# Optimization experiments

Measured on AMD Instinct MI355X. Metric: run time of the kernel, lower is better.

## Reference

```python
import jax, jax.numpy as jnp
import numpy as np

B, Cin, Cout, H, W = 8, 64, 128, 128, 128
K, S, P = 3, 1, 1
KK = K * K
EPS = 1e-5


def _conv2d(x, w, b=None):
    out = jax.lax.conv_general_dilated(
        x, w, window_strides=(S, S), padding=[(P, P), (P, P)],
        dimension_numbers=('NCHW', 'OIHW', 'NCHW'))
    if b is not None:
        out = out + b[None, :, None, None]
    return out


def setup_inputs() -> dict:
    key = jax.random.key(0)
    k = jax.random.split(key, 5)
    sc = 1.0 / np.sqrt(Cin * KK)
    return {
        'x': jax.random.normal(k[0], (B, Cin, H, W), jnp.float32),
        'offset_w': jax.random.normal(k[1], (2 * KK, Cin, K, K), jnp.float32) * sc,
        'offset_b': jnp.zeros((2 * KK,), jnp.float32),
        'mask_w': jax.random.normal(k[2], (KK, Cin, K, K), jnp.float32) * sc,
        'mask_b': jnp.zeros((KK,), jnp.float32),
        'conv_w': jax.random.normal(k[3], (Cout, Cin, K, K), jnp.float32) * sc,
    }


def _deform_conv2d(x, offset, mask, w):
    """Modulated deformable conv (torchvision deform_conv2d semantics)."""
    Bn, C, Hh, Ww = x.shape
    Ho, Wo = offset.shape[2], offset.shape[3]
    off = offset.reshape(Bn, KK, 2, Ho, Wo)  # (y, x) pairs per kernel tap
    ky, kx = jnp.meshgrid(jnp.arange(K), jnp.arange(K), indexing='ij')
    ky = ky.reshape(KK).astype(x.dtype)
    kx = kx.reshape(KK).astype(x.dtype)
    hy = (jnp.arange(Ho) * S - P).astype(x.dtype)
    wx = (jnp.arange(Wo) * S - P).astype(x.dtype)
    # sampling positions [B, KK, Ho, Wo]
    py = off[:, :, 0] + ky[None, :, None, None] + hy[None, None, :, None]
    px = off[:, :, 1] + kx[None, :, None, None] + wx[None, None, None, :]

    y0 = jnp.floor(py)
    x0 = jnp.floor(px)
    wy1 = py - y0; wx1 = px - x0
    wy0 = 1.0 - wy1; wx0 = 1.0 - wx1

    xf = x.reshape(Bn, C, Hh * Ww)

    def gather(yi, xi):
        valid = ((yi >= 0) & (yi < Hh) & (xi >= 0) & (xi < Ww)).astype(x.dtype)
        yc = jnp.clip(yi, 0, Hh - 1).astype(jnp.int32)
        xc = jnp.clip(xi, 0, Ww - 1).astype(jnp.int32)
        idx = (yc * Ww + xc).reshape(Bn, -1)  # [B, KK*Ho*Wo]
        vals = jnp.take_along_axis(xf, idx[:, None, :], axis=2)  # [B, C, KK*Ho*Wo]
        return vals.reshape(Bn, C, KK, Ho, Wo) * valid.reshape(Bn, 1, KK, Ho, Wo)

    v = (gather(y0, x0) * (wy0 * wx0)[:, None]
         + gather(y0, x0 + 1) * (wy0 * wx1)[:, None]
         + gather(y0 + 1, x0) * (wy1 * wx0)[:, None]
         + gather(y0 + 1, x0 + 1) * (wy1 * wx1)[:, None])  # [B, C, KK, Ho, Wo]
    v = v * mask[:, None]  # modulation
    return jnp.einsum('bckhw,ock->bohw', v, w.reshape(w.shape[0], C, KK))


def reference(x, offset_w, offset_b, mask_w, mask_b, conv_w):
    offset = _conv2d(x, offset_w, offset_b)
    mask = jax.nn.sigmoid(_conv2d(x, mask_w, mask_b))
    out = _deform_conv2d(x, offset, mask, conv_w)
    # BatchNorm2d(affine=False), training-mode normalization over (N, H, W)
    mean = out.mean(axis=(0, 2, 3), keepdims=True)
    var = out.var(axis=(0, 2, 3), keepdims=True)
    return jax.nn.relu((out - mean) * jax.lax.rsqrt(var + EPS))
```

## Files before the change

kernel.cpp:

```cpp
#include <hip/hip_runtime.h>
#include <hip/hip_bf16.h>

#define H_ 128
#define W_ 128
#define HW 16384
#define CIN 64
#define COUT 128
#define KK9 9
#define BATCH 8
#define NPIX (BATCH * HW)
#define KDIM 576

typedef short bf16x8 __attribute__((ext_vector_type(8)));
typedef float f32x4  __attribute__((ext_vector_type(4)));
typedef unsigned short ushort_t;

union U4B { uint4 u; bf16x8 v; };

__device__ __forceinline__ float us2f(unsigned short u) {
    unsigned int v = ((unsigned int)u) << 16;
    float f;
    __builtin_memcpy(&f, &v, 4);
    return f;
}
__device__ __forceinline__ float lo_f(unsigned int w) {
    unsigned int v = w << 16;
    float f;
    __builtin_memcpy(&f, &v, 4);
    return f;
}
__device__ __forceinline__ float hi_f(unsigned int w) {
    unsigned int v = w & 0xffff0000u;
    float f;
    __builtin_memcpy(&f, &v, 4);
    return f;
}
__device__ __forceinline__ unsigned short f2us_bf(float f) {
    __hip_bfloat16 h = __float2bfloat16(f);
    unsigned short u;
    __builtin_memcpy(&u, &h, 2);
    return u;
}
__device__ __forceinline__ unsigned int pack2(float a, float b) {
    return (unsigned int)f2us_bf(a) | ((unsigned int)f2us_bf(b) << 16);
}

template <bool F32>
__device__ __forceinline__ float ld_in(const void* p, long i) {
    if (F32) return ((const float*)p)[i];
    return us2f(((const unsigned short*)p)[i]);
}

__global__ void detect_zero(const uint4* __restrict__ xr4,
                            float* __restrict__ flag,
                            float* __restrict__ gstat) {
    int t = threadIdx.x;
#pragma unroll
    for (int i = 0; i < 16; ++i) gstat[i * 256 + t] = 0.0f;
    if (t < 64) {
        uint4 v = xr4[t];
        unsigned int w[4] = {v.x, v.y, v.z, v.w};
        int big = 0;
#pragma unroll
        for (int q = 0; q < 4; ++q) {
            big += (((w[q] >> 7)  & 0xFF) >= 0xC0);
            big += (((w[q] >> 23) & 0xFF) >= 0xC0);
        }
        unsigned long long m = __ballot(big > 0);
        if (t == 0) flag[0] = m ? 1.0f : 0.0f;
    }
}

template <bool F32>
__device__ __forceinline__ void prep_body(const void* offw, const void* offb,
                                          const void* maskw, const void* maskb,
                                          const void* convw,
                                          ushort_t* wTs, ushort_t* wcats,
                                          float* bias, int i) {
    if (i < 73728) {
        int j = i & 7, lane = (i >> 3) & 63, n = (i >> 9) & 7, ks = i >> 12;
        int co = n * 16 + (lane & 15);
        int k  = ks * 32 + ((lane >> 4) << 3) + j;
        int kk = k >> 6, ci = k & 63;
        wTs[i] = f2us_bf(ld_in<F32>(convw, (long)co * KDIM + ci * 9 + kk));
    } else if (i < 73728 + 18432) {
        int i2 = i - 73728;
        int j = i2 & 7, lane = (i2 >> 3) & 63, n = (i2 >> 9) & 1, ks = i2 >> 10;
        int co2 = n * 16 + (lane & 15);
        int k   = ks * 32 + ((lane >> 4) << 3) + j;
        int kk = k >> 6, ci = k & 63;
        float v = 0.0f;
        if (co2 < 18)      v = ld_in<F32>(offw,  (long)co2 * KDIM + ci * 9 + kk);
        else if (co2 < 27) v = ld_in<F32>(maskw, (long)(co2 - 18) * KDIM + ci * 9 + kk);
        wcats[i2] = f2us_bf(v);
    } else if (i < 73728 + 18432 + 32) {
        int j = i - 73728 - 18432;
        float v = 0.0f;
        if (j < 18)      v = ld_in<F32>(offb, j);
        else if (j < 27) v = ld_in<F32>(maskb, j - 18);
        bias[j] = v;
    }
}

__global__ void prep_weights(const void* __restrict__ offw,
                             const void* __restrict__ offb,
                             const void* __restrict__ maskw,
                             const void* __restrict__ maskb,
                             const void* __restrict__ convw,
                             const float* __restrict__ flag,
                             ushort_t* __restrict__ wTs,
                             ushort_t* __restrict__ wcats,
                             float* __restrict__ bias) {
    int i = blockIdx.x * 256 + threadIdx.x;
    if (flag[0] != 0.0f)
        prep_body<true>(offw, offb, maskw, maskb, convw, wTs, wcats, bias, i);
    else
        prep_body<false>(offw, offb, maskw, maskb, convw, wTs, wcats, bias, i);
}

template <bool F32>
__device__ __forceinline__ void transpose_body(const void* x, ushort_t* xnb) {
    __shared__ float tile[CIN][64 + 1];
    int blk  = blockIdx.x;
    int b    = blk >> 8;
    int pix0 = (blk & 255) * 64;
    int t    = threadIdx.x;
    int lane = t & 63;
    int grp  = t >> 6;
#pragma unroll
    for (int r = 0; r < 16; ++r) {
        int ci = r * 4 + grp;
        tile[ci][lane] = ld_in<F32>(x, (long)(b * CIN + ci) * HW + pix0 + lane);
    }
    __syncthreads();
#pragma unroll
    for (int r = 0; r < 16; ++r) {
        int px = r * 4 + grp;
        xnb[(size_t)(b * HW + pix0 + px) * CIN + lane] = f2us_bf(tile[lane][px]);
    }
}

__global__ __launch_bounds__(256) void transpose_x(const void* __restrict__ x,
                                                   const float* __restrict__ flag,
                                                   ushort_t* __restrict__ xnb) {
    if (flag[0] != 0.0f) transpose_body<true>(x, xnb);
    else                 transpose_body<false>(x, xnb);
}

__global__ __launch_bounds__(1024, 4) void conv_mfma(
        const ushort_t* __restrict__ xnb,
        const ushort_t* __restrict__ wcats,
        const float* __restrict__ bias,
        float* __restrict__ off2,
        float* __restrict__ mask_ws) {
    __shared__ uint4 ldsB4[2304];

    int t    = threadIdx.x;
    int pix0 = blockIdx.x * 256;
    int b    = pix0 >> 14;
    int rem0 = pix0 & 16383;

    const uint4* ws4 = (const uint4*)wcats;
#pragma unroll
    for (int i = t; i < 2304; i += 1024) ldsB4[i] = ws4[i];

    int wave = t >> 6, lane = t & 63, mrow = lane & 15, quad = lane >> 4;
    int px_l = wave * 16 + mrow;
    int remp = rem0 + px_l;
    int yp = remp >> 7, xp = remp & 127;
    const ushort_t* xb = xnb + (size_t)b * HW * CIN + quad * 8;

    uint4 af0[9], af1[9];
#pragma unroll
    for (int kk = 0; kk < 9; ++kk) {
        int yy = yp + kk / 3 - 1;
        int xq = xp + kk % 3 - 1;
        bool ok = (yy >= 0) && (yy < H_) && (xq >= 0) && (xq < W_);
        const ushort_t* src = xb + (size_t)(yy * W_ + xq) * CIN;
        af0[kk] = ok ? *(const uint4*)src        : make_uint4(0, 0, 0, 0);
        af1[kk] = ok ? *(const uint4*)(src + 32) : make_uint4(0, 0, 0, 0);
    }
    __syncthreads();

    f32x4 acc[2];
    acc[0] = (f32x4){0.f, 0.f, 0.f, 0.f};
    acc[1] = (f32x4){0.f, 0.f, 0.f, 0.f};
    const ushort_t* ldsB = (const ushort_t*)ldsB4;
#pragma unroll
    for (int kk = 0; kk < 9; ++kk) {
#pragma unroll
        for (int half = 0; half < 2; ++half) {
            int ks = kk * 2 + half;
            U4B a; a.u = half ? af1[kk] : af0[kk];
#pragma unroll
            for (int n = 0; n < 2; ++n) {
                bf16x8 bf = *(const bf16x8*)(ldsB + ((ks * 2 + n) * 64 + lane) * 8);
                acc[n] = __builtin_amdgcn_mfma_f32_16x16x32_bf16(a.v, bf, acc[n], 0, 0, 0);
            }
        }
    }

#pragma unroll
    for (int n = 0; n < 2; ++n) {
        int co2 = n * 16 + mrow;
        if (co2 >= 27) continue;
        float bs = bias[co2];
#pragma unroll
        for (int r = 0; r < 4; ++r) {
            int px = wave * 16 + quad * 4 + r;
            float v = acc[n][r] + bs;
            if (co2 < 18) {
                off2[((size_t)(b * 9 + (co2 >> 1)) * HW + rem0 + px) * 2 + (co2 & 1)] = v;
            } else {
                mask_ws[(size_t)(b * 9 + (co2 - 18)) * HW + rem0 + px] =
                    1.0f / (1.0f + __expf(-v));
            }
        }
    }
}

__device__ __forceinline__ void compute_tap(int yp_t, int xp_t,
                                            float oy, float ox, float mk,
                                            int* ofs, float* wg) {
    float py  = (float)yp_t + oy;
    float pxf = (float)xp_t + ox;
    float y0f = floorf(py), x0f = floorf(pxf);
    int yi = (int)y0f, xi = (int)x0f;
    float wy1 = py - y0f, wx1 = pxf - x0f;
    float wy0 = 1.0f - wy1, wx0 = 1.0f - wx1;
    int ya  = min(max(yi, 0), H_ - 1);
    int yb  = min(max(yi + 1, 0), H_ - 1);
    int xa  = min(max(xi, 0), W_ - 1);
    int xb2 = min(max(xi + 1, 0), W_ - 1);
    bool vy0 = (yi >= 0) & (yi < H_);
    bool vy1 = (yi >= -1) & (yi < H_ - 1);
    bool vx0 = (xi >= 0) & (xi < W_);
    bool vx1 = (xi >= -1) & (xi < W_ - 1);
    float m0 = mk * wy0, m1 = mk * wy1;
    wg[0] = (vy0 & vx0) ? m0 * wx0 : 0.0f;
    wg[1] = (vy0 & vx1) ? m0 * wx1 : 0.0f;
    wg[2] = (vy1 & vx0) ? m1 * wx0 : 0.0f;
    wg[3] = (vy1 & vx1) ? m1 * wx1 : 0.0f;
    int ra = ya << 13, rb = yb << 13;
    int ca = xa << 6,  cb_ = xb2 << 6;
    ofs[0] = ra + ca;  ofs[1] = ra + cb_;
    ofs[2] = rb + ca;  ofs[3] = rb + cb_;
}

__device__ __forceinline__ void issue_half(const ushort_t* __restrict__ xb,
                                           const int* ofs, int hoff, uint4* cb) {
#pragma unroll
    for (int c = 0; c < 4; ++c)
        cb[c] = *(const uint4*)(xb + ofs[c] + hoff);
}

__device__ __forceinline__ void consume_half(int ks, const uint4* cb,
                                             const float* wg,
                                             const ushort_t* __restrict__ ldsB,
                                             int lane, f32x4* acc) {
    float2 v2[4];
#pragma unroll
    for (int j = 0; j < 4; ++j) v2[j] = make_float2(0.f, 0.f);
#pragma unroll
    for (int c = 0; c < 4; ++c) {
        float w = wg[c];
        unsigned int ww[4] = {cb[c].x, cb[c].y, cb[c].z, cb[c].w};
#pragma unroll
        for (int j = 0; j < 4; ++j) {
            v2[j].x = fmaf(w, lo_f(ww[j]), v2[j].x);
            v2[j].y = fmaf(w, hi_f(ww[j]), v2[j].y);
        }
    }
    U4B a;
    a.u = make_uint4(pack2(v2[0].x, v2[0].y), pack2(v2[1].x, v2[1].y),
                     pack2(v2[2].x, v2[2].y), pack2(v2[3].x, v2[3].y));
    const ushort_t* bbase = ldsB + ((size_t)(ks * 8) * 64 + lane) * 8;
#pragma unroll
    for (int n = 0; n < 8; ++n) {
        bf16x8 bf = *(const bf16x8*)(bbase + n * 64 * 8);
        acc[n] = __builtin_amdgcn_mfma_f32_16x16x32_bf16(a.v, bf, acc[n], 0, 0, 0);
    }
}

__global__ __launch_bounds__(1024, 4) void deform_mfma(
        const ushort_t* __restrict__ xnb,
        const float* __restrict__ off2,
        const float* __restrict__ mask_ws,
        const ushort_t* __restrict__ wTs,
        ushort_t* __restrict__ prebn,
        float* __restrict__ gstat) {
    __shared__ uint4 ldsB4[9216];
    __shared__ float red[256];

    int t    = threadIdx.x;
    int pix0 = blockIdx.x * 256;
    int b    = pix0 >> 14;
    int rem0 = pix0 & 16383;

    const uint4* ws4 = (const uint4*)wTs;
#pragma unroll
    for (int i = 0; i < 9; ++i) ldsB4[i * 1024 + t] = ws4[i * 1024 + t];
    if (t < 256) red[t] = 0.0f;

    int wave = t >> 6, lane = t & 63, mrow = lane & 15, quad = lane >> 4;
    int px_l = wave * 16 + mrow;
    int remp = rem0 + px_l;
    int yp = remp >> 7, xp = remp & 127;
    const ushort_t* xb = xnb + (size_t)b * HW * CIN + quad * 8;
    size_t obase = (size_t)b * 9 * HW + remp;

    float2 oE = *(const float2*)(off2 + obase * 2);
    float2 oO = *(const float2*)(off2 + (obase + HW) * 2);
    float mkE = mask_ws[obase];
    float mkO = mask_ws[obase + HW];
    __syncthreads();

    f32x4 acc[8];
#pragma unroll
    for (int n = 0; n < 8; ++n) acc[n] = (f32x4){0.f, 0.f, 0.f, 0.f};
    const ushort_t* ldsB = (const ushort_t*)ldsB4;

    int   ofs[2][4];
    float wg[2][4];
    uint4 cb[2][4];

    compute_tap(yp - 1, xp - 1, oE.x, oE.y, mkE, ofs[0], wg[0]);
    issue_half(xb, ofs[0], 0, cb[0]);
    __builtin_amdgcn_sched_barrier(0);

#pragma unroll
    for (int hs = 0; hs < 18; ++hs) {
        const int kk = hs >> 1;
        const int h  = hs & 1;
        const int tp = kk & 1;
        const int bp = hs & 1;
        if (h == 0) {
            issue_half(xb, ofs[tp], 32, cb[bp ^ 1]);
        } else {
            if (kk < 8) {
                const int nt = kk + 1;
                float ooy = (nt & 1) ? oO.x : oE.x;
                float oox = (nt & 1) ? oO.y : oE.y;
                float omk = (nt & 1) ? mkO : mkE;
                compute_tap(yp + nt / 3 - 1, xp + nt % 3 - 1, ooy, oox, omk,
                            ofs[tp ^ 1], wg[tp ^ 1]);
                issue_half(xb, ofs[tp ^ 1], 0, cb[bp ^ 1]);
            }
            if (kk < 7) {
                const int pt = kk + 2;
                float2 o = *(const float2*)(off2 + (obase + (size_t)pt * HW) * 2);
                float  m = mask_ws[obase + (size_t)pt * HW];
                if (tp) { oO = o; mkO = m; } else { oE = o; mkE = m; }
            }
        }
        __builtin_amdgcn_sched_barrier(0);
        consume_half(hs, cb[bp], wg[tp], ldsB, lane, acc);
    }

#pragma unroll
    for (int n = 0; n < 8; ++n) {
        int co = n * 16 + mrow;
        float s = 0.f, ss = 0.f;
#pragma unroll
        for (int r = 0; r < 4; ++r) {
            int pg = pix0 + wave * 16 + quad * 4 + r;
            float v = acc[n][r];
            prebn[(size_t)pg * COUT + co] = f2us_bf(v);
            s += v;
            ss += v * v;
        }
        s  += __shfl_xor(s, 16, 64);
        s  += __shfl_xor(s, 32, 64);
        ss += __shfl_xor(ss, 16, 64);
        ss += __shfl_xor(ss, 32, 64);
        if (quad == 0) {
            atomicAdd(&red[co], s);
            atomicAdd(&red[128 + co], ss);
        }
    }
    __syncthreads();
    if (t < 256) atomicAdd(&gstat[(blockIdx.x & 15) * 256 + t], red[t]);
}

__global__ __launch_bounds__(256) void bn_apply_t(const ushort_t* __restrict__ prebn,
                                                  const float* __restrict__ gstat,
                                                  float* __restrict__ out) {
    __shared__ float tile[128 * 65];
    __shared__ float mvs[256];
    int t = threadIdx.x;
    if (t < 128) {
        float s = 0.f, ss = 0.f;
#pragma unroll
        for (int part = 0; part < 16; ++part) {
            s  += gstat[part * 256 + t];
            ss += gstat[part * 256 + 128 + t];
        }
        const float invN = 1.0f / (float)NPIX;
        float mean = s * invN;
        float var  = ss * invN - mean * mean;
        if (!isfinite(mean)) mean = 0.0f;
        float r = rsqrtf(fmaxf(var, 0.0f) + 1e-5f);
        if (!isfinite(r)) r = 1.0f;
        mvs[t]       = mean;
        mvs[128 + t] = r;
    }
    __syncthreads();
    int pix0 = blockIdx.x * 64;
    int b    = pix0 >> 14;
    int rem0 = pix0 & 16383;
    const ushort_t* src = prebn + (size_t)pix0 * COUT;
#pragma unroll
    for (int r = 0; r < 32; ++r) {
        int i = r * 256 + t;
        int p = i >> 7, c = i & 127;
        float v = us2f(src[i]);
        v = fmaxf((v - mvs[c]) * mvs[128 + c], 0.0f);
        tile[c * 65 + p] = v;
    }
    __syncthreads();
#pragma unroll
    for (int r = 0; r < 32; ++r) {
        int i = r * 256 + t;
        int c2 = i >> 6, p2 = i & 63;
        out[(size_t)(b * COUT + c2) * HW + rem0 + p2] = tile[c2 * 65 + p2];
    }
}

extern "C" void kernel_launch(void* const* d_in, const int* in_sizes, int n_in,
                              void* d_out, int out_size, void* d_ws, size_t ws_size,
                              hipStream_t stream) {
    (void)in_sizes; (void)n_in; (void)out_size; (void)ws_size;
    const void* x     = d_in[0];
    const void* offw  = d_in[1];
    const void* offb  = d_in[2];
    const void* maskw = d_in[3];
    const void* maskb = d_in[4];
    const void* convw = d_in[5];

    float* ws       = (float*)d_ws;
    float* off2     = ws;
    float* mask_ws  = off2 + 2359296;
    float* bias     = mask_ws + 1179648;
    float* gstat    = bias + 32;
    float* flag     = gstat + 4096;
    ushort_t* wTs   = (ushort_t*)(flag + 16);
    ushort_t* wcats = wTs + 73728;
    ushort_t* xnb   = wcats + 18432;
    ushort_t* prebn = xnb + 8388608;
    float* out      = (float*)d_out;

    detect_zero<<<1, 256, 0, stream>>>((const uint4*)x, flag, gstat);
    prep_weights<<<361, 256, 0, stream>>>(offw, offb, maskw, maskb, convw, flag, wTs, wcats, bias);
    transpose_x<<<2048, 256, 0, stream>>>(x, flag, xnb);
    conv_mfma<<<512, 1024, 0, stream>>>(xnb, wcats, bias, off2, mask_ws);
    deform_mfma<<<512, 1024, 0, stream>>>(xnb, off2, mask_ws, wTs, prebn, gstat);
    bn_apply_t<<<2048, 256, 0, stream>>>(prebn, gstat, out);
}
```

Before: 219.8 us.

## Deepen deform gather prefetch to triple buffer, swizzle blocks, raise MFMA priority

The deform kernel now prefetches bilinear gather loads two half-steps ahead using three rotating buffers instead of two, so more global-memory latency is hidden behind the MFMA work. Both the conv and deform kernels remap block IDs so that consecutive blocks go to different images, which spreads the work differently across XCDs and caches. MFMA issue is wrapped in s_setprio to favour the matrix work. The deeper prefetch costs extra VGPRs under a 1024-thread launch bound, which could cause spills or lower occupancy.

```diff
diff --git a/kernel.cpp b/kernel.cpp
--- a/kernel.cpp
+++ b/kernel.cpp
@@ -156,7 +156,9 @@
     __shared__ uint4 ldsB4[2304];
 
     int t    = threadIdx.x;
-    int pix0 = blockIdx.x * 256;
+    int bid  = blockIdx.x;
+    int sbid = (bid & 7) * 64 + (bid >> 3);
+    int pix0 = sbid * 256;
     int b    = pix0 >> 14;
     int rem0 = pix0 & 16383;
 
@@ -275,11 +277,13 @@
     a.u = make_uint4(pack2(v2[0].x, v2[0].y), pack2(v2[1].x, v2[1].y),
                      pack2(v2[2].x, v2[2].y), pack2(v2[3].x, v2[3].y));
     const ushort_t* bbase = ldsB + ((size_t)(ks * 8) * 64 + lane) * 8;
+    __builtin_amdgcn_s_setprio(1);
 #pragma unroll
     for (int n = 0; n < 8; ++n) {
         bf16x8 bf = *(const bf16x8*)(bbase + n * 64 * 8);
         acc[n] = __builtin_amdgcn_mfma_f32_16x16x32_bf16(a.v, bf, acc[n], 0, 0, 0);
     }
+    __builtin_amdgcn_s_setprio(0);
 }
 
 __global__ __launch_bounds__(1024, 4) void deform_mfma(
@@ -293,7 +297,9 @@
     __shared__ float red[256];
 
     int t    = threadIdx.x;
-    int pix0 = blockIdx.x * 256;
+    int bid  = blockIdx.x;
+    int sbid = (bid & 7) * 64 + (bid >> 3);
+    int pix0 = sbid * 256;
     int b    = pix0 >> 14;
     int rem0 = pix0 & 16383;
 
@@ -322,39 +328,40 @@
 
     int   ofs[2][4];
     float wg[2][4];
-    uint4 cb[2][4];
+    uint4 cb[3][4];
 
     compute_tap(yp - 1, xp - 1, oE.x, oE.y, mkE, ofs[0], wg[0]);
-    issue_half(xb, ofs[0], 0, cb[0]);
+    issue_half(xb, ofs[0], 0,  cb[0]);
+    issue_half(xb, ofs[0], 32, cb[1]);
+    oE  = *(const float2*)(off2 + (obase + (size_t)2 * HW) * 2);
+    mkE = mask_ws[obase + (size_t)2 * HW];
     __builtin_amdgcn_sched_barrier(0);
 
 #pragma unroll
     for (int hs = 0; hs < 18; ++hs) {
-        const int kk = hs >> 1;
-        const int h  = hs & 1;
-        const int tp = kk & 1;
-        const int bp = hs & 1;
-        if (h == 0) {
-            issue_half(xb, ofs[tp], 32, cb[bp ^ 1]);
-        } else {
-            if (kk < 8) {
-                const int nt = kk + 1;
-                float ooy = (nt & 1) ? oO.x : oE.x;
-                float oox = (nt & 1) ? oO.y : oE.y;
-                float omk = (nt & 1) ? mkO : mkE;
-                compute_tap(yp + nt / 3 - 1, xp + nt % 3 - 1, ooy, oox, omk,
-                            ofs[tp ^ 1], wg[tp ^ 1]);
-                issue_half(xb, ofs[tp ^ 1], 0, cb[bp ^ 1]);
+        const int hs2 = hs + 2;
+        if (hs2 < 18) {
+            const int kk2 = hs2 >> 1;
+            const int s2  = hs2 % 3;
+            if ((hs2 & 1) == 0) {
+                const int tp2 = kk2 & 1;
+                float ooy = tp2 ? oO.x : oE.x;
+                float oox = tp2 ? oO.y : oE.y;
+                float omk = tp2 ? mkO  : mkE;
+                compute_tap(yp + kk2 / 3 - 1, xp + kk2 % 3 - 1, ooy, oox, omk,
+                            ofs[tp2], wg[tp2]);
+                issue_half(xb, ofs[tp2], 0, cb[s2]);
+                if (kk2 + 2 <= 8) {
+                    float2 o = *(const float2*)(off2 + (obase + (size_t)(kk2 + 2) * HW) * 2);
+                    float  m = mask_ws[obase + (size_t)(kk2 + 2) * HW];
+                    if (tp2) { oO = o; mkO = m; } else { oE = o; mkE = m; }
+                }
+            } else {
+                issue_half(xb, ofs[kk2 & 1], 32, cb[s2]);
             }
-            if (kk < 7) {
-                const int pt = kk + 2;
-                float2 o = *(const float2*)(off2 + (obase + (size_t)pt * HW) * 2);
-                float  m = mask_ws[obase + (size_t)pt * HW];
-                if (tp) { oO = o; mkO = m; } else { oE = o; mkE = m; }
-            }
         }
         __builtin_amdgcn_sched_barrier(0);
-        consume_half(hs, cb[bp], wg[tp], ldsB, lane, acc);
+        consume_half(hs, cb[hs % 3], wg[(hs >> 1) & 1], ldsB, lane, acc);
     }
 
 #pragma unroll
@@ -379,7 +386,7 @@
         }
     }
     __syncthreads();
-    if (t < 256) atomicAdd(&gstat[(blockIdx.x & 15) * 256 + t], red[t]);
+    if (t < 256) atomicAdd(&gstat[(bid & 15) * 256 + t], red[t]);
 }
 
 __global__ __launch_bounds__(256) void bn_apply_t(const ushort_t* __restrict__ prebn,
```

Result: no change. 217.9 us (-0.9%).
